# Kernel tuning notes

Measured on AMD Instinct MI355X. Metric: run time of the kernel, lower is better.

## Reference

```python
import jax, jax.numpy as jnp
import numpy as np
from jax import lax

B, NBB, C, H, W = 32, 16, 1024, 22, 22
P = 3            # pooled output size (3x3)
SCALE = 1.0 / 16.0
EPS = 1e-5


def setup_inputs() -> dict:
    key = jax.random.key(0)
    ks = jax.random.split(key, 12)
    feat = jax.random.normal(ks[0], (B, C, H, W), jnp.float32)
    # bbox in xywh image coords, in-range for a 352x352 search region
    xy = jax.random.uniform(ks[1], (B, NBB, 2), jnp.float32, 0.0, 250.0)
    wh = jax.random.uniform(ks[2], (B, NBB, 2), jnp.float32, 16.0, 100.0)
    bbox = jnp.concatenate([xy, wh], axis=-1)
    conv_w = jax.random.normal(ks[3], (C, C, 3, 3), jnp.float32) * 0.01
    conv_b = jnp.zeros((C,), jnp.float32)
    bn_gamma = jnp.ones((C,), jnp.float32)
    bn_beta = jnp.zeros((C,), jnp.float32)
    bn_mean = jax.random.normal(ks[4], (C,), jnp.float32) * 0.1
    bn_var = jax.random.uniform(ks[5], (C,), jnp.float32, 0.5, 1.5)
    w1 = jax.random.normal(ks[6], (C // 2, C), jnp.float32) * 0.02
    b1 = jnp.zeros((C // 2,), jnp.float32)
    w2 = jax.random.normal(ks[7], (C // 2, C // 2), jnp.float32) * 0.02
    b2 = jnp.zeros((C // 2,), jnp.float32)
    w3 = jax.random.normal(ks[8], (512, C // 2), jnp.float32) * 0.02
    b3 = jnp.zeros((512,), jnp.float32)
    return dict(feat=feat, bbox=bbox, conv_w=conv_w, conv_b=conv_b,
                bn_gamma=bn_gamma, bn_beta=bn_beta, bn_mean=bn_mean, bn_var=bn_var,
                w1=w1, b1=b1, w2=w2, b2=b2, w3=w3, b3=b3)


def _hat_int(t):
    # Antiderivative of the bilinear hat h(u)=max(0,1-|u|), clipped to support.
    t = jnp.clip(t, -1.0, 1.0)
    return t + 0.5 - 0.5 * t * jnp.abs(t)


def _bin_weights(lo, bw, n):
    # lo, bw: [B, NBB].  Returns exact integral weights [B, NBB, P, n]:
    # W[b,r,p,i] = integral over bin p of hat(x - i) dx  (PrRoI closed form).
    p = jnp.arange(P, dtype=lo.dtype)
    xs = lo[..., None] + p * bw[..., None]          # [B,NBB,P] bin starts
    xe = xs + bw[..., None]                          # bin ends
    i = jnp.arange(n, dtype=lo.dtype)
    return _hat_int(xe[..., None] - i) - _hat_int(xs[..., None] - i)


def reference(feat, bbox, conv_w, conv_b, bn_gamma, bn_beta, bn_mean, bn_var,
              w1, b1, w2, b2, w3, b3):
    # --- PrRoI pooling (exact separable bilinear integral) ---
    x1 = bbox[..., 0] * SCALE
    y1 = bbox[..., 1] * SCALE
    x2 = (bbox[..., 0] + bbox[..., 2]) * SCALE
    y2 = (bbox[..., 1] + bbox[..., 3]) * SCALE
    bw = (x2 - x1) / P
    bh = (y2 - y1) / P
    Wx = _bin_weights(x1, bw, W)                     # [B,NBB,P,W]
    Wy = _bin_weights(y1, bh, H)                     # [B,NBB,P,H]
    pooled = jnp.einsum('bchw,bnqh,bnpw->bncqp', feat, Wy, Wx)  # [B,NBB,C,P,P]
    area = jnp.maximum(bw * bh, 0.0)[..., None, None, None]
    pooled = jnp.where(area > 0, pooled / jnp.maximum(area, 1e-12), 0.0)
    x = pooled.reshape(B * NBB, C, P, P)

    # --- conv_bn_relu: 3x3 conv, valid padding -> 1x1, BN (eval), ReLU ---
    x = lax.conv_general_dilated(x, conv_w, (1, 1), 'VALID',
                                 dimension_numbers=('NCHW', 'OIHW', 'NCHW'))
    x = x + conv_b[:, None, None]
    x = (x - bn_mean[:, None, None]) * (bn_gamma * lax.rsqrt(bn_var + EPS))[:, None, None]
    x = x + bn_beta[:, None, None]
    x = jax.nn.relu(x)

    # --- MLP head ---
    x = x.reshape(B * NBB, C)
    x = jax.nn.relu(x @ w1.T + b1)
    x = jax.nn.relu(x @ w2.T + b2)
    x = x @ w3.T + b3
    return x.reshape(B, NBB, 512)
```

## Files before the change

kernel.cpp:

```cpp
#include <hip/hip_runtime.h>
#include <hip/hip_bf16.h>

#define B_    32
#define NBB_  16
#define C_    1024
#define H_    22
#define W_    22
#define NROI  512
#define KCONV 9216
#define SCALE_ (1.0f/16.0f)
#define EPS_  1e-5f

using f32x4  = __attribute__((ext_vector_type(4))) float;
using bf16x8 = __attribute__((ext_vector_type(8))) short;

__device__ __forceinline__ unsigned short f2bf(float f) {
  union { float f; unsigned u; } x; x.f = f;
  unsigned r = x.u + 0x7fffu + ((x.u >> 16) & 1u);
  return (unsigned short)(r >> 16);
}

__device__ __forceinline__ float hat_int(float t) {
  t = fminf(fmaxf(t, -1.f), 1.f);
  return t + 0.5f - 0.5f * t * fabsf(t);
}

__device__ __forceinline__ void glds16(const void* g, void* l) {
  __builtin_amdgcn_global_load_lds((const __attribute__((address_space(1))) void*)g,
                                   (__attribute__((address_space(3))) void*)l, 16, 0, 0);
}

__global__ __launch_bounds__(32) void prep_rois(const float* __restrict__ bbox,
                                                float* __restrict__ wy,
                                                float* __restrict__ wx) {
  int r = blockIdx.x;
  float4 bb = ((const float4*)bbox)[r];
  float x1 = bb.x * SCALE_, y1 = bb.y * SCALE_;
  float x2 = (bb.x + bb.z) * SCALE_, y2 = (bb.y + bb.w) * SCALE_;
  float bw = (x2 - x1) / 3.f, bh = (y2 - y1) / 3.f;
  float area = fmaxf(bw * bh, 0.f);
  float inv = area > 0.f ? 1.f / fmaxf(area, 1e-12f) : 0.f;
  int i = threadIdx.x;
  if (i < 22) {
    float fi = (float)i;
#pragma unroll
    for (int q = 0; q < 3; ++q) {
      float sy = y1 + q * bh;
      wy[r*66 + q*22 + i] = hat_int(sy + bh - fi) - hat_int(sy - fi);
      float sx = x1 + q * bw;
      wx[r*66 + q*22 + i] = (hat_int(sx + bw - fi) - hat_int(sx - fi)) * inv;
    }
  }
}

__global__ __launch_bounds__(256) void cvt_bf16(const float* __restrict__ src,
                                                unsigned short* __restrict__ dst, int n8) {
  int i = blockIdx.x * 256 + threadIdx.x;
  if (i >= n8) return;
  float4 a = ((const float4*)src)[2*i];
  float4 b = ((const float4*)src)[2*i + 1];
  uint4 pk;
  pk.x = (unsigned)f2bf(a.x) | ((unsigned)f2bf(a.y) << 16);
  pk.y = (unsigned)f2bf(a.z) | ((unsigned)f2bf(a.w) << 16);
  pk.z = (unsigned)f2bf(b.x) | ((unsigned)f2bf(b.y) << 16);
  pk.w = (unsigned)f2bf(b.z) | ((unsigned)f2bf(b.w) << 16);
  ((uint4*)dst)[i] = pk;
}

__global__ __launch_bounds__(192) void pool_mfma(const float* __restrict__ feat,
                                                 const float* __restrict__ wyg,
                                                 const float* __restrict__ wxg,
                                                 unsigned short* __restrict__ X) {
  __shared__ __align__(16) unsigned short A[22*16*40];
  __shared__ __align__(16) unsigned short Bx[48*32];
  __shared__ float wyS[16*66];
  int tid = threadIdx.x;
  int cb = blockIdx.x, b = blockIdx.y;

  const float4* f4 = (const float4*)(feat + ((size_t)b * C_ + (size_t)cb * 16) * 484);
  for (int i = tid; i < 1936; i += 192) {
    float4 v = f4[i];
    int lin = i * 4;
    {
      int c = lin / 484, rem = lin - c * 484, h = rem / 22, w = rem - h * 22;
      unsigned pk = (unsigned)f2bf(v.x) | ((unsigned)f2bf(v.y) << 16);
      *(unsigned*)&A[(h*16 + c)*40 + w] = pk;
    }
    {
      int lin2 = lin + 2;
      int c = lin2 / 484, rem = lin2 - c * 484, h = rem / 22, w = rem - h * 22;
      unsigned pk = (unsigned)f2bf(v.z) | ((unsigned)f2bf(v.w) << 16);
      *(unsigned*)&A[(h*16 + c)*40 + w] = pk;
    }
  }
  for (int z = tid; z < 352*5; z += 192) {
    int row = z / 5, j = z - row * 5;
    *(unsigned*)&A[row*40 + 22 + j*2] = 0u;
  }
  if (tid < 48) {
    int n = tid / 3, p = tid - n * 3;
    const float* wxp = wxg + ((size_t)b * 16 + n) * 66 + p * 22;
#pragma unroll
    for (int w = 0; w < 22; w += 2) {
      unsigned pk = (unsigned)f2bf(wxp[w]) | ((unsigned)f2bf(wxp[w+1]) << 16);
      *(unsigned*)&Bx[tid*32 + w] = pk;
    }
#pragma unroll
    for (int w = 22; w < 32; w += 2) *(unsigned*)&Bx[tid*32 + w] = 0u;
  }
  for (int i = tid; i < 1056; i += 192) wyS[i] = wyg[(size_t)b * 1056 + i];
  __syncthreads();

  int lane = tid & 63, wid = tid >> 6;
  int l15 = lane & 15, kg = lane >> 4;
  int np = wid * 16 + l15;
  int n = np / 3, p = np - n * 3;
  bf16x8 bfrag = *(const bf16x8*)&Bx[np*32 + kg*8];
  const float* wyp = wyS + n * 66;
  const unsigned short* Abase = A + l15*40 + kg*8;

  f32x4 zero = {};
  f32x4 acc0 = {}, acc1 = {}, acc2 = {};
  bf16x8 a0 = *(const bf16x8*)&Abase[0];
  f32x4 t0 = __builtin_amdgcn_mfma_f32_16x16x32_bf16(a0, bfrag, zero, 0, 0, 0);
#pragma unroll
  for (int h = 0; h < 21; ++h) {
    bf16x8 a1 = *(const bf16x8*)&Abase[(h+1)*640];
    f32x4 t1 = __builtin_amdgcn_mfma_f32_16x16x32_bf16(a1, bfrag, zero, 0, 0, 0);
    acc0 += t0 * wyp[h];
    acc1 += t0 * wyp[22 + h];
    acc2 += t0 * wyp[44 + h];
    t0 = t1;
  }
  acc0 += t0 * wyp[21];
  acc1 += t0 * wyp[43];
  acc2 += t0 * wyp[65];

  unsigned short* xrow = X + ((size_t)b*16 + n) * KCONV + (size_t)cb * 144;
#pragma unroll
  for (int r = 0; r < 4; ++r) {
    int base = (kg*4 + r) * 9 + p;
    xrow[base]     = f2bf(acc0[r]);
    xrow[base + 3] = f2bf(acc1[r]);
    xrow[base + 6] = f2bf(acc2[r]);
  }
}

__global__ __launch_bounds__(256) void gemm128(const unsigned short* __restrict__ A,
                                               const unsigned short* __restrict__ Bm,
                                               float* __restrict__ Cp,
                                               int M, int N, int K, int kChunk) {
  __shared__ __align__(16) unsigned short As[2][4096];
  __shared__ __align__(16) unsigned short Bs[2][4096];
  int tid = threadIdx.x;
  int lane = tid & 63, wid = tid >> 6;
  int wm = wid >> 1, wn = wid & 1;
  int l15 = lane & 15, kg = lane >> 4;
  int nt = blockIdx.x, mt = blockIdx.y, z = blockIdx.z;
  int kbeg = z * kChunk;
  int steps = kChunk / 32;

  int row0 = tid >> 2, row1 = 64 + row0;
  int slot = tid & 3;
  int s0 = slot ^ ((row0 >> 1) & 3);
  int s1 = slot ^ ((row1 >> 1) & 3);
  const unsigned short* ga0 = A  + (size_t)(mt*128 + row0) * K + kbeg + s0*8;
  const unsigned short* ga1 = A  + (size_t)(mt*128 + row1) * K + kbeg + s1*8;
  const unsigned short* gb0 = Bm + (size_t)(nt*128 + row0) * K + kbeg + s0*8;
  const unsigned short* gb1 = Bm + (size_t)(nt*128 + row1) * K + kbeg + s1*8;
  int wbyte = wid * 1024;

  f32x4 acc[4][4] = {};
  int cur = 0;

#define ISSUE(buf, s) do { int ko = (s) * 32; \
    glds16(ga0 + ko, (char*)&As[(buf)][0] + wbyte); \
    glds16(ga1 + ko, (char*)&As[(buf)][0] + 4096 + wbyte); \
    glds16(gb0 + ko, (char*)&Bs[(buf)][0] + wbyte); \
    glds16(gb1 + ko, (char*)&Bs[(buf)][0] + 4096 + wbyte); } while (0)

  ISSUE(0, 0);
  for (int s = 0; s < steps; ++s) {
    __syncthreads();
    if (s + 1 < steps) ISSUE(cur ^ 1, s + 1);
    bf16x8 af[4], bfr[4];
#pragma unroll
    for (int fm = 0; fm < 4; ++fm) {
      int fr = wm*64 + fm*16 + l15;
      af[fm] = *(const bf16x8*)&As[cur][fr*32 + ((kg ^ ((fr >> 1) & 3)) << 3)];
    }
#pragma unroll
    for (int fn = 0; fn < 4; ++fn) {
      int fr = wn*64 + fn*16 + l15;
      bfr[fn] = *(const bf16x8*)&Bs[cur][fr*32 + ((kg ^ ((fr >> 1) & 3)) << 3)];
    }
#pragma unroll
    for (int fm = 0; fm < 4; ++fm)
#pragma unroll
      for (int fn = 0; fn < 4; ++fn)
        acc[fm][fn] = __builtin_amdgcn_mfma_f32_16x16x32_bf16(af[fm], bfr[fn], acc[fm][fn], 0, 0, 0);
    cur ^= 1;
  }
#undef ISSUE

  float* cp = Cp + ((size_t)z * M + (size_t)mt * 128) * N + (size_t)nt * 128;
#pragma unroll
  for (int fm = 0; fm < 4; ++fm)
#pragma unroll
    for (int fn = 0; fn < 4; ++fn)
#pragma unroll
      for (int r = 0; r < 4; ++r) {
        int row = wm*64 + fm*16 + kg*4 + r;
        int col = wn*64 + fn*16 + l15;
        cp[(size_t)row * N + col] = acc[fm][fn][r];
      }
}

__global__ __launch_bounds__(256) void gemm_nt(const unsigned short* __restrict__ A,
                                               const unsigned short* __restrict__ Bm,
                                               float* __restrict__ Cp,
                                               int M, int N, int K, int kChunk) {
  __shared__ __align__(16) unsigned short As[64][40];
  __shared__ __align__(16) unsigned short Bs[64][40];
  int tid = threadIdx.x;
  int lane = tid & 63, wid = tid >> 6;
  int wm = wid >> 1, wn = wid & 1;
  int l15 = lane & 15, kg = lane >> 4;
  int nt = blockIdx.x, mt = blockIdx.y, z = blockIdx.z;
  int kbeg = z * kChunk;
  int kend = kbeg + kChunk; if (kend > K) kend = K;
  int srow = tid >> 2, sseg = tid & 3;
  const unsigned short* aG = A  + (size_t)(mt*64 + srow) * K + sseg * 8;
  const unsigned short* bG = Bm + (size_t)(nt*64 + srow) * K + sseg * 8;
  f32x4 acc[2][2] = {};

  for (int k0 = kbeg; k0 < kend; k0 += 32) {
    uint4 av = *(const uint4*)(aG + k0);
    uint4 bv = *(const uint4*)(bG + k0);
    __syncthreads();
    *(uint4*)&As[srow][sseg*8] = av;
    *(uint4*)&Bs[srow][sseg*8] = bv;
    __syncthreads();
    bf16x8 a0 = *(const bf16x8*)&As[wm*32 +      l15][kg*8];
    bf16x8 a1 = *(const bf16x8*)&As[wm*32 + 16 + l15][kg*8];
    bf16x8 b0 = *(const bf16x8*)&Bs[wn*32 +      l15][kg*8];
    bf16x8 b1 = *(const bf16x8*)&Bs[wn*32 + 16 + l15][kg*8];
    acc[0][0] = __builtin_amdgcn_mfma_f32_16x16x32_bf16(a0, b0, acc[0][0], 0, 0, 0);
    acc[0][1] = __builtin_amdgcn_mfma_f32_16x16x32_bf16(a0, b1, acc[0][1], 0, 0, 0);
    acc[1][0] = __builtin_amdgcn_mfma_f32_16x16x32_bf16(a1, b0, acc[1][0], 0, 0, 0);
    acc[1][1] = __builtin_amdgcn_mfma_f32_16x16x32_bf16(a1, b1, acc[1][1], 0, 0, 0);
  }

  float* cp = Cp + ((size_t)z * M + (size_t)mt * 64) * N + (size_t)nt * 64;
#pragma unroll
  for (int fm = 0; fm < 2; ++fm)
#pragma unroll
    for (int fn = 0; fn < 2; ++fn)
#pragma unroll
      for (int r = 0; r < 4; ++r) {
        int row = wm*32 + fm*16 + kg*4 + r;
        int col = wn*32 + fn*16 + l15;
        cp[(size_t)row * N + col] = acc[fm][fn][r];
      }
}

template<int MODE>
__global__ __launch_bounds__(256) void epi(const float* __restrict__ Cp, int SK, int MN4, int N,
                                           const float* __restrict__ bias,
                                           const float* __restrict__ g,
                                           const float* __restrict__ be,
                                           const float* __restrict__ mu,
                                           const float* __restrict__ var,
                                           unsigned short* __restrict__ outb,
                                           float* __restrict__ outf) {
  int i = blockIdx.x * 256 + threadIdx.x;
  if (i >= MN4) return;
  float4 s = ((const float4*)Cp)[i];
  for (int z = 1; z < SK; ++z) {
    float4 t = ((const float4*)Cp)[(size_t)z * MN4 + i];
    s.x += t.x; s.y += t.y; s.z += t.z; s.w += t.w;
  }
  int n0 = (i * 4) % N;
  float v[4] = {s.x, s.y, s.z, s.w};
  if (MODE == 0) {
    unsigned short o[4];
#pragma unroll
    for (int j = 0; j < 4; ++j) {
      int n = n0 + j;
      float sc = g[n] * rsqrtf(var[n] + EPS_);
      float t = (v[j] + bias[n] - mu[n]) * sc + be[n];
      o[j] = f2bf(fmaxf(t, 0.f));
    }
    uint2 pk; pk.x = (unsigned)o[0] | ((unsigned)o[1] << 16);
    pk.y = (unsigned)o[2] | ((unsigned)o[3] << 16);
    *(uint2*)&outb[(size_t)i * 4] = pk;
  } else if (MODE == 1) {
    unsigned short o[4];
#pragma unroll
    for (int j = 0; j < 4; ++j) o[j] = f2bf(fmaxf(v[j] + bias[n0 + j], 0.f));
    uint2 pk; pk.x = (unsigned)o[0] | ((unsigned)o[1] << 16);
    pk.y = (unsigned)o[2] | ((unsigned)o[3] << 16);
    *(uint2*)&outb[(size_t)i * 4] = pk;
  } else {
    float4 o;
    o.x = v[0] + bias[n0];     o.y = v[1] + bias[n0 + 1];
    o.z = v[2] + bias[n0 + 2]; o.w = v[3] + bias[n0 + 3];
    ((float4*)outf)[i] = o;
  }
}

extern "C" void kernel_launch(void* const* d_in, const int* in_sizes, int n_in,
                              void* d_out, int out_size, void* d_ws, size_t ws_size,
                              hipStream_t stream) {
  const float* feat   = (const float*)d_in[0];
  const float* bbox   = (const float*)d_in[1];
  const float* conv_w = (const float*)d_in[2];
  const float* conv_b = (const float*)d_in[3];
  const float* gamma  = (const float*)d_in[4];
  const float* beta   = (const float*)d_in[5];
  const float* mean   = (const float*)d_in[6];
  const float* var    = (const float*)d_in[7];
  const float* w1     = (const float*)d_in[8];
  const float* b1     = (const float*)d_in[9];
  const float* w2     = (const float*)d_in[10];
  const float* b2     = (const float*)d_in[11];
  const float* w3     = (const float*)d_in[12];
  const float* b3     = (const float*)d_in[13];

  char* ws = (char*)d_ws;
  float*          wy  = (float*)(ws);
  float*          wx  = (float*)(ws + 135168);
  unsigned short* Xb  = (unsigned short*)(ws + 270336);
  unsigned short* Wfb = (unsigned short*)(ws + 9707520);
  unsigned short* w1b = (unsigned short*)(ws + 28581888);
  unsigned short* w2b = (unsigned short*)(ws + 29630464);
  unsigned short* w3b = (unsigned short*)(ws + 30154752);
  float*          part= (float*)(ws + 30679040);
  unsigned short* H0  = (unsigned short*)(ws + 47456256);
  unsigned short* H1  = (unsigned short*)(ws + 48504832);
  unsigned short* H2  = (unsigned short*)(ws + 49029120);

  prep_rois<<<NROI, 32, 0, stream>>>(bbox, wy, wx);
  cvt_bf16<<<(1179648 + 255) / 256, 256, 0, stream>>>(conv_w, Wfb, 1179648);
  cvt_bf16<<<(65536 + 255) / 256, 256, 0, stream>>>(w1, w1b, 65536);
  cvt_bf16<<<(32768 + 255) / 256, 256, 0, stream>>>(w2, w2b, 32768);
  cvt_bf16<<<(32768 + 255) / 256, 256, 0, stream>>>(w3, w3b, 32768);
  pool_mfma<<<dim3(64, 32), 192, 0, stream>>>(feat, wy, wx, Xb);

  gemm128<<<dim3(8, 4, 8), 256, 0, stream>>>(Xb, Wfb, part, 512, 1024, 9216, 1152);
  epi<0><<<(131072 + 255) / 256, 256, 0, stream>>>(part, 8, 131072, 1024,
      conv_b, gamma, beta, mean, var, H0, nullptr);

  gemm_nt<<<dim3(8, 8, 4), 256, 0, stream>>>(H0, w1b, part, 512, 512, 1024, 256);
  epi<1><<<(65536 + 255) / 256, 256, 0, stream>>>(part, 4, 65536, 512,
      b1, nullptr, nullptr, nullptr, nullptr, H1, nullptr);

  gemm_nt<<<dim3(8, 8, 4), 256, 0, stream>>>(H1, w2b, part, 512, 512, 512, 128);
  epi<1><<<(65536 + 255) / 256, 256, 0, stream>>>(part, 4, 65536, 512,
      b2, nullptr, nullptr, nullptr, nullptr, H2, nullptr);

  gemm_nt<<<dim3(8, 8, 4), 256, 0, stream>>>(H2, w3b, part, 512, 512, 512, 128);
  epi<2><<<(65536 + 255) / 256, 256, 0, stream>>>(part, 4, 65536, 512,
      b3, nullptr, nullptr, nullptr, nullptr, nullptr, (float*)d_out);
}
```

Measured before the change: 117.5 us.

## Recast PrRoI pooling as a per-image GEMM with precomputed 2D weights

Separable pooling (an MFMA over width then an FMA scan over height) is replaced by building a full 2D bin-weight matrix per image (144x512 bf16) and running a tiled MFMA GEMM against the bf16 feature map. The output layout of X is changed to qp-major (qp*1024 + channel), and conv weights are transposed to match in a new convw_t kernel. The conv GEMM split-K goes from 8 to 6 chunks. This aims to raise MFMA utilisation in pooling, at the cost of computing over the padded 512-length K and rounding the wy*wx products to bf16.

```diff
diff --git a/kernel.cpp b/kernel.cpp
--- a/kernel.cpp
+++ b/kernel.cpp
@@ -4,8 +4,6 @@
 #define B_    32
 #define NBB_  16
 #define C_    1024
-#define H_    22
-#define W_    22
 #define NROI  512
 #define KCONV 9216
 #define SCALE_ (1.0f/16.0f)
@@ -14,10 +12,10 @@
 using f32x4  = __attribute__((ext_vector_type(4))) float;
 using bf16x8 = __attribute__((ext_vector_type(8))) short;
 
-__device__ __forceinline__ unsigned short f2bf(float f) {
+__device__ __forceinline__ unsigned f2bf(float f) {
   union { float f; unsigned u; } x; x.f = f;
   unsigned r = x.u + 0x7fffu + ((x.u >> 16) & 1u);
-  return (unsigned short)(r >> 16);
+  return r >> 16;
 }
 
 __device__ __forceinline__ float hat_int(float t) {
@@ -60,90 +58,126 @@
   float4 a = ((const float4*)src)[2*i];
   float4 b = ((const float4*)src)[2*i + 1];
   uint4 pk;
-  pk.x = (unsigned)f2bf(a.x) | ((unsigned)f2bf(a.y) << 16);
-  pk.y = (unsigned)f2bf(a.z) | ((unsigned)f2bf(a.w) << 16);
-  pk.z = (unsigned)f2bf(b.x) | ((unsigned)f2bf(b.y) << 16);
-  pk.w = (unsigned)f2bf(b.z) | ((unsigned)f2bf(b.w) << 16);
+  pk.x = f2bf(a.x) | (f2bf(a.y) << 16);
+  pk.y = f2bf(a.z) | (f2bf(a.w) << 16);
+  pk.z = f2bf(b.x) | (f2bf(b.y) << 16);
+  pk.w = f2bf(b.z) | (f2bf(b.w) << 16);
   ((uint4*)dst)[i] = pk;
 }
 
-__global__ __launch_bounds__(192) void pool_mfma(const float* __restrict__ feat,
-                                                 const float* __restrict__ wyg,
-                                                 const float* __restrict__ wxg,
+__global__ __launch_bounds__(256) void convw_t(const float* __restrict__ cw,
+                                               unsigned short* __restrict__ out) {
+  __shared__ float T[9][260];
+  int o = blockIdx.x, cc = blockIdx.y;
+  int tid = threadIdx.x;
+  const float* src = cw + (size_t)o * 9216 + (size_t)cc * 2304;
+  for (int i = tid; i < 576; i += 256) {
+    float4 v = ((const float4*)src)[i];
+    int e = i * 4;
+#pragma unroll
+    for (int j = 0; j < 4; ++j) {
+      int ee = e + j;
+      int c = ee / 9, qp = ee - c * 9;
+      T[qp][c] = ((const float*)&v)[j];
+    }
+  }
+  __syncthreads();
+  unsigned short* dst = out + (size_t)o * 9216 + cc * 256 + tid;
+#pragma unroll
+  for (int qp = 0; qp < 9; ++qp) dst[qp * 1024] = (unsigned short)f2bf(T[qp][tid]);
+}
+
+__global__ __launch_bounds__(192) void w2d_build(const float* __restrict__ wy,
+                                                 const float* __restrict__ wx,
+                                                 unsigned short* __restrict__ W2d) {
+  __shared__ float wyS[1056], wxS[1056];
+  int b = blockIdx.x, tid = threadIdx.x;
+  for (int i = tid; i < 1056; i += 192) { wyS[i] = wy[(size_t)b*1056 + i]; wxS[i] = wx[(size_t)b*1056 + i]; }
+  __syncthreads();
+  if (tid < 144) {
+    int n = tid / 9, qp = tid - n*9, q = qp / 3, p = qp - q*3;
+    const float* wyp = wyS + n*66 + q*22;
+    const float* wxp = wxS + n*66 + p*22;
+    unsigned short* out = W2d + ((size_t)b*144 + tid) * 512;
+    for (int h = 0; h < 22; ++h) {
+      float yv = wyp[h];
+      int kb = h * 22;
+#pragma unroll
+      for (int w = 0; w < 22; w += 2) {
+        unsigned pk = f2bf(yv * wxp[w]) | (f2bf(yv * wxp[w+1]) << 16);
+        *(unsigned*)&out[kb + w] = pk;
+      }
+    }
+    for (int k = 484; k < 512; k += 2) *(unsigned*)&out[k] = 0u;
+  }
+}
+
+__global__ __launch_bounds__(384) void pool_gemm(const float* __restrict__ feat,
+                                                 const unsigned short* __restrict__ W2d,
                                                  unsigned short* __restrict__ X) {
-  __shared__ __align__(16) unsigned short A[22*16*40];
-  __shared__ __align__(16) unsigned short Bx[48*32];
-  __shared__ float wyS[16*66];
+  __shared__ __align__(16) unsigned short As[144 * 72];
+  __shared__ __align__(16) unsigned short Bs[64 * 72];
   int tid = threadIdx.x;
-  int cb = blockIdx.x, b = blockIdx.y;
-
-  const float4* f4 = (const float4*)(feat + ((size_t)b * C_ + (size_t)cb * 16) * 484);
-  for (int i = tid; i < 1936; i += 192) {
-    float4 v = f4[i];
-    int lin = i * 4;
-    {
-      int c = lin / 484, rem = lin - c * 484, h = rem / 22, w = rem - h * 22;
-      unsigned pk = (unsigned)f2bf(v.x) | ((unsigned)f2bf(v.y) << 16);
-      *(unsigned*)&A[(h*16 + c)*40 + w] = pk;
-    }
-    {
-      int lin2 = lin + 2;
-      int c = lin2 / 484, rem = lin2 - c * 484, h = rem / 22, w = rem - h * 22;
-      unsigned pk = (unsigned)f2bf(v.z) | ((unsigned)f2bf(v.w) << 16);
-      *(unsigned*)&A[(h*16 + c)*40 + w] = pk;
-    }
-  }
-  for (int z = tid; z < 352*5; z += 192) {
-    int row = z / 5, j = z - row * 5;
-    *(unsigned*)&A[row*40 + 22 + j*2] = 0u;
-  }
-  if (tid < 48) {
-    int n = tid / 3, p = tid - n * 3;
-    const float* wxp = wxg + ((size_t)b * 16 + n) * 66 + p * 22;
-#pragma unroll
-    for (int w = 0; w < 22; w += 2) {
-      unsigned pk = (unsigned)f2bf(wxp[w]) | ((unsigned)f2bf(wxp[w+1]) << 16);
-      *(unsigned*)&Bx[tid*32 + w] = pk;
-    }
-#pragma unroll
-    for (int w = 22; w < 32; w += 2) *(unsigned*)&Bx[tid*32 + w] = 0u;
-  }
-  for (int i = tid; i < 1056; i += 192) wyS[i] = wyg[(size_t)b * 1056 + i];
-  __syncthreads();
-
+  int nch = blockIdx.x, b = blockIdx.y;
   int lane = tid & 63, wid = tid >> 6;
+  int wm = wid >> 1, wn = wid & 1;
   int l15 = lane & 15, kg = lane >> 4;
-  int np = wid * 16 + l15;
-  int n = np / 3, p = np - n * 3;
-  bf16x8 bfrag = *(const bf16x8*)&Bx[np*32 + kg*8];
-  const float* wyp = wyS + n * 66;
-  const unsigned short* Abase = A + l15*40 + kg*8;
-
-  f32x4 zero = {};
-  f32x4 acc0 = {}, acc1 = {}, acc2 = {};
-  bf16x8 a0 = *(const bf16x8*)&Abase[0];
-  f32x4 t0 = __builtin_amdgcn_mfma_f32_16x16x32_bf16(a0, bfrag, zero, 0, 0, 0);
-#pragma unroll
-  for (int h = 0; h < 21; ++h) {
-    bf16x8 a1 = *(const bf16x8*)&Abase[(h+1)*640];
-    f32x4 t1 = __builtin_amdgcn_mfma_f32_16x16x32_bf16(a1, bfrag, zero, 0, 0, 0);
-    acc0 += t0 * wyp[h];
-    acc1 += t0 * wyp[22 + h];
-    acc2 += t0 * wyp[44 + h];
-    t0 = t1;
-  }
-  acc0 += t0 * wyp[21];
-  acc1 += t0 * wyp[43];
-  acc2 += t0 * wyp[65];
-
-  unsigned short* xrow = X + ((size_t)b*16 + n) * KCONV + (size_t)cb * 144;
-#pragma unroll
-  for (int r = 0; r < 4; ++r) {
-    int base = (kg*4 + r) * 9 + p;
-    xrow[base]     = f2bf(acc0[r]);
-    xrow[base + 3] = f2bf(acc1[r]);
-    xrow[base + 6] = f2bf(acc2[r]);
-  }
+  const unsigned short* w2b = W2d + (size_t)b * 144 * 512;
+  const float* fb = feat + ((size_t)b * C_ + (size_t)nch * 64) * 484;
+  f32x4 acc[3][2] = {};
+
+  for (int s = 0; s < 8; ++s) {
+    __syncthreads();
+#pragma unroll
+    for (int t = 0; t < 3; ++t) {
+      int i = tid + t * 384;
+      int row = i >> 3, slot = i & 7;
+      uint4 v = *(const uint4*)(w2b + (size_t)row * 512 + s * 64 + slot * 8);
+      *(uint4*)&As[row * 72 + slot * 8] = v;
+    }
+    for (int i = tid; i < 1024; i += 384) {
+      int c = i >> 4, f4 = i & 15;
+      float4 v;
+      if (s < 7 || f4 <= 8) v = *(const float4*)(fb + (size_t)c * 484 + s * 64 + f4 * 4);
+      else v = make_float4(0.f, 0.f, 0.f, 0.f);
+      uint2 pk;
+      pk.x = f2bf(v.x) | (f2bf(v.y) << 16);
+      pk.y = f2bf(v.z) | (f2bf(v.w) << 16);
+      *(uint2*)&Bs[c * 72 + f4 * 4] = pk;
+    }
+    __syncthreads();
+
+    bf16x8 af[3][2], bf[2][2];
+#pragma unroll
+    for (int fm = 0; fm < 3; ++fm)
+#pragma unroll
+      for (int kk = 0; kk < 2; ++kk)
+        af[fm][kk] = *(const bf16x8*)&As[(wm*48 + fm*16 + l15) * 72 + kk*32 + kg*8];
+#pragma unroll
+    for (int fn = 0; fn < 2; ++fn)
+#pragma unroll
+      for (int kk = 0; kk < 2; ++kk)
+        bf[fn][kk] = *(const bf16x8*)&Bs[(wn*32 + fn*16 + l15) * 72 + kk*32 + kg*8];
+#pragma unroll
+    for (int fm = 0; fm < 3; ++fm)
+#pragma unroll
+      for (int fn = 0; fn < 2; ++fn) {
+        acc[fm][fn] = __builtin_amdgcn_mfma_f32_16x16x32_bf16(af[fm][0], bf[fn][0], acc[fm][fn], 0, 0, 0);
+        acc[fm][fn] = __builtin_amdgcn_mfma_f32_16x16x32_bf16(af[fm][1], bf[fn][1], acc[fm][fn], 0, 0, 0);
+      }
+  }
+
+#pragma unroll
+  for (int fm = 0; fm < 3; ++fm)
+#pragma unroll
+    for (int r = 0; r < 4; ++r) {
+      int m = wm*48 + fm*16 + kg*4 + r;
+      int n = m / 9, qp = m - n*9;
+      size_t base = ((size_t)(b*16 + n)) * KCONV + (size_t)qp * 1024 + (size_t)nch * 64;
+#pragma unroll
+      for (int fn = 0; fn < 2; ++fn)
+        X[base + wn*32 + fn*16 + l15] = (unsigned short)f2bf(acc[fm][fn][r]);
+    }
 }
 
 __global__ __launch_bounds__(256) void gemm128(const unsigned short* __restrict__ A,
@@ -283,7 +317,7 @@
   int n0 = (i * 4) % N;
   float v[4] = {s.x, s.y, s.z, s.w};
   if (MODE == 0) {
-    unsigned short o[4];
+    unsigned o[4];
 #pragma unroll
     for (int j = 0; j < 4; ++j) {
       int n = n0 + j;
@@ -291,15 +325,13 @@
       float t = (v[j] + bias[n] - mu[n]) * sc + be[n];
       o[j] = f2bf(fmaxf(t, 0.f));
     }
-    uint2 pk; pk.x = (unsigned)o[0] | ((unsigned)o[1] << 16);
-    pk.y = (unsigned)o[2] | ((unsigned)o[3] << 16);
+    uint2 pk; pk.x = o[0] | (o[1] << 16); pk.y = o[2] | (o[3] << 16);
     *(uint2*)&outb[(size_t)i * 4] = pk;
   } else if (MODE == 1) {
-    unsigned short o[4];
+    unsigned o[4];
 #pragma unroll
     for (int j = 0; j < 4; ++j) o[j] = f2bf(fmaxf(v[j] + bias[n0 + j], 0.f));
-    uint2 pk; pk.x = (unsigned)o[0] | ((unsigned)o[1] << 16);
-    pk.y = (unsigned)o[2] | ((unsigned)o[3] << 16);
+    uint2 pk; pk.x = o[0] | (o[1] << 16); pk.y = o[2] | (o[3] << 16);
     *(uint2*)&outb[(size_t)i * 4] = pk;
   } else {
     float4 o;
@@ -330,25 +362,28 @@
   char* ws = (char*)d_ws;
   float*          wy  = (float*)(ws);
   float*          wx  = (float*)(ws + 135168);
-  unsigned short* Xb  = (unsigned short*)(ws + 270336);
-  unsigned short* Wfb = (unsigned short*)(ws + 9707520);
-  unsigned short* w1b = (unsigned short*)(ws + 28581888);
-  unsigned short* w2b = (unsigned short*)(ws + 29630464);
-  unsigned short* w3b = (unsigned short*)(ws + 30154752);
-  float*          part= (float*)(ws + 30679040);
-  unsigned short* H0  = (unsigned short*)(ws + 47456256);
-  unsigned short* H1  = (unsigned short*)(ws + 48504832);
-  unsigned short* H2  = (unsigned short*)(ws + 49029120);
+  unsigned short* W2d = (unsigned short*)(ws + 270336);
+  unsigned short* H0  = (unsigned short*)(ws);
+  unsigned short* H1  = (unsigned short*)(ws + 1048576);
+  unsigned short* H2  = (unsigned short*)(ws + 1572864);
+  unsigned short* Xb  = (unsigned short*)(ws + 4988928);
+  unsigned short* Wfb = (unsigned short*)(ws + 14426112);
+  unsigned short* w1b = (unsigned short*)(ws + 33300480);
+  unsigned short* w2b = (unsigned short*)(ws + 34349056);
+  unsigned short* w3b = (unsigned short*)(ws + 34873344);
+  float*          part= (float*)(ws + 35397632);
 
   prep_rois<<<NROI, 32, 0, stream>>>(bbox, wy, wx);
-  cvt_bf16<<<(1179648 + 255) / 256, 256, 0, stream>>>(conv_w, Wfb, 1179648);
+  w2d_build<<<32, 192, 0, stream>>>(wy, wx, W2d);
+  convw_t<<<dim3(1024, 4), 256, 0, stream>>>(conv_w, Wfb);
   cvt_bf16<<<(65536 + 255) / 256, 256, 0, stream>>>(w1, w1b, 65536);
   cvt_bf16<<<(32768 + 255) / 256, 256, 0, stream>>>(w2, w2b, 32768);
   cvt_bf16<<<(32768 + 255) / 256, 256, 0, stream>>>(w3, w3b, 32768);
-  pool_mfma<<<dim3(64, 32), 192, 0, stream>>>(feat, wy, wx, Xb);
-
-  gemm128<<<dim3(8, 4, 8), 256, 0, stream>>>(Xb, Wfb, part, 512, 1024, 9216, 1152);
-  epi<0><<<(131072 + 255) / 256, 256, 0, stream>>>(part, 8, 131072, 1024,
+
+  pool_gemm<<<dim3(16, 32), 384, 0, stream>>>(feat, W2d, Xb);
+
+  gemm128<<<dim3(8, 4, 6), 256, 0, stream>>>(Xb, Wfb, part, 512, 1024, 9216, 1536);
+  epi<0><<<(131072 + 255) / 256, 256, 0, stream>>>(part, 6, 131072, 1024,
       conv_b, gamma, beta, mean, var, H0, nullptr);
 
   gemm_nt<<<dim3(8, 8, 4), 256, 0, stream>>>(H0, w1b, part, 512, 512, 1024, 256);
```

Result: slower. 134.5 us (+14.5%).
